# Kernel tuning notes

Measured on AMD Instinct MI355X. Metric: run time of the kernel, lower is better.

The kernel has to match this reference:

```python
import jax, jax.numpy as jnp
import numpy as np

N_DOF = 7
WIDTH = 1024
BATCH = 8192
EPS = 1e-5
LSIZE = N_DOF * (N_DOF + 1) // 2   # diag (n) + strictly-lower ((n^2-n)/2)


def _tri_idx(n):
    # order matches LowTri: offset -i chunks, within-chunk j -> entry (j+i, j)
    r, c = [], []
    for i in range(n):
        for j in range(n - i):
            r.append(j + i)
            c.append(j)
    return np.array(r, np.int32), np.array(c, np.int32)

_R, _C = _tri_idx(N_DOF)


def setup_inputs() -> dict:
    key = jax.random.key(0)
    ks = jax.random.split(key, 9)

    def glorot(k, shape):
        std = (2.0 / (shape[0] + shape[1])) ** 0.5
        return (jax.random.normal(k, shape, jnp.float32) * std).astype(jnp.float32)

    lower = LSIZE - N_DOF
    b0 = 0.1
    return {
        "state": jax.random.normal(ks[0], (BATCH, N_DOF), jnp.float32),
        "velocity": jax.random.normal(ks[1], (BATCH, N_DOF), jnp.float32),
        "acceleration": jax.random.normal(ks[2], (BATCH, N_DOF), jnp.float32),
        "W_in": glorot(ks[3], (N_DOF, WIDTH)), "b_in": jnp.full((WIDTH,), b0, jnp.float32),
        "W_h": glorot(ks[4], (WIDTH, WIDTH)), "b_h": jnp.full((WIDTH,), b0, jnp.float32),
        "W_g": glorot(ks[5], (WIDTH, 1)), "b_g": jnp.full((1,), b0, jnp.float32),
        "W_ld": glorot(ks[6], (WIDTH, N_DOF)), "b_ld": jnp.full((N_DOF,), b0, jnp.float32),
        "W_lo": glorot(ks[7], (WIDTH, lower)), "b_lo": jnp.full((lower,), b0, jnp.float32),
    }


def _layer(x, der, W, b, act):
    # a: [B, out]; der: [B, in, n_dof] -> [B, out, n_dof]
    a = x @ W + b
    if act == "relu":
        y = jax.nn.relu(a)
        gp = (a > 0).astype(a.dtype)
    else:  # linear
        y = a
        gp = jnp.ones_like(a)
    # diag(g'(a)) @ W^T @ prev_der  ==  g'(a)[:, :, None] * (W^T @ prev_der)
    new_der = gp[:, :, None] * jnp.einsum("io,bid->bod", W, der)
    return y, new_der


def _forward(state, velocity, acceleration,
             W_in, b_in, W_h, b_h, W_g, b_g, W_ld, b_ld, W_lo, b_lo):
    B = state.shape[0]
    eye = jnp.broadcast_to(jnp.eye(N_DOF, dtype=state.dtype), (B, N_DOF, N_DOF))

    y1, d1 = _layer(state, eye, W_in, b_in, "relu")
    y2, d2 = _layer(y1, d1, W_h, b_h, "relu")
    y3, d3 = _layer(y2, d2, W_h, b_h, "relu")   # original reuses hidden_layer1 twice

    V, derV = _layer(y3, d3, W_g, b_g, "linear")       # derV: [B, 1, n_dof]
    l_diag, der_ld = _layer(y3, d3, W_ld, b_ld, "relu")
    l_low, der_lo = _layer(y3, d3, W_lo, b_lo, "linear")

    l = jnp.concatenate([l_diag, l_low], axis=1)          # [B, LSIZE]
    der_l = jnp.concatenate([der_ld, der_lo], axis=1)     # [B, LSIZE, n_dof]

    def lowtri(v):   # [B, LSIZE] -> [B, n, n]
        return jnp.zeros((B, N_DOF, N_DOF), v.dtype).at[:, _R, _C].set(v)

    def lowtri3d(v):  # [B, n_dof, LSIZE] -> [B, n_dof, n, n]
        return jnp.zeros((B, N_DOF, N_DOF, N_DOF), v.dtype).at[:, :, _R, _C].set(v)

    L = lowtri(l)
    LT = jnp.swapaxes(L, 1, 2)
    M = L @ LT + EPS * jnp.eye(N_DOF, dtype=L.dtype)

    dldt = jnp.einsum("bld,bd->bl", der_l, velocity)
    dLdt = lowtri(dldt)
    dMdt = L @ jnp.swapaxes(dLdt, 1, 2) + dLdt @ LT

    dLdq = lowtri3d(jnp.swapaxes(der_l, 1, 2))            # [B, n_dof, n, n]
    dMdq = dLdq @ LT[:, None] + L[:, None] @ jnp.swapaxes(dLdq, 2, 3)

    dMdt_dq = jnp.einsum("bij,bj->bi", dMdt, velocity)
    quad_dq = jnp.einsum("bi,bkij,bj->bk", velocity, dMdq, velocity)
    C = dMdt_dq - 0.5 * quad_dq
    G = derV[:, 0, :]                                      # squeeze [B,1,n_dof]
    Mddq = jnp.einsum("bij,bj->bi", M, acceleration)
    tau_pred = Mddq + C + G
    return tau_pred, M, C, G


def reference(state, velocity, acceleration,
              W_in, b_in, W_h, b_h, W_g, b_g, W_ld, b_ld, W_lo, b_lo):
    return _forward(state, velocity, acceleration,
                    W_in, b_in, W_h, b_h, W_g, b_g, W_ld, b_ld, W_lo, b_lo)
```

## Files before the change

### kernel.cpp

```cpp
#include <hip/hip_runtime.h>
#include <hip/hip_bf16.h>

#define WIDTH 1024
#define BATCH 8192

typedef __attribute__((ext_vector_type(8))) short short8;
typedef __attribute__((ext_vector_type(4))) float floatx4;

typedef __attribute__((address_space(1))) void gvoid;
typedef __attribute__((address_space(3))) void lvoid;

__device__ __forceinline__ void async_copy16(const void* g, void* l) {
    __builtin_amdgcn_global_load_lds((gvoid*)g, (lvoid*)l, 16, 0, 0);
}

__device__ __forceinline__ void split_store(float v, __hip_bfloat16* hi, __hip_bfloat16* lo, long idx) {
    __hip_bfloat16 h = __float2bfloat16(v);
    hi[idx] = h;
    lo[idx] = __float2bfloat16(v - __bfloat162float(h));
}

__global__ __launch_bounds__(256) void transpose_k(
    const float* __restrict__ W,
    __hip_bfloat16* __restrict__ Wth, __hip_bfloat16* __restrict__ Wtl)
{
    __shared__ float t[32][33];
    const int tx = threadIdx.x & 31, ty = threadIdx.x >> 5;
    const int bx = blockIdx.x << 5, by = blockIdx.y << 5;
#pragma unroll
    for (int r = 0; r < 32; r += 8)
        t[ty + r][tx] = W[(long)(by + ty + r) * WIDTH + bx + tx];
    __syncthreads();
#pragma unroll
    for (int r = 0; r < 32; r += 8)
        split_store(t[tx][ty + r], Wth, Wtl, (long)(bx + ty + r) * WIDTH + by + tx);
}

__global__ __launch_bounds__(256) void buildwcat_k(
    const float* __restrict__ W_ld, const float* __restrict__ W_lo,
    const float* __restrict__ W_g,
    __hip_bfloat16* __restrict__ Wch, __hip_bfloat16* __restrict__ Wcl)
{
    const int idx = blockIdx.x * 256 + threadIdx.x;
    const int n = idx >> 10, k = idx & 1023;
    float v = 0.f;
    if (n < 7)       v = W_ld[k * 7 + n];
    else if (n < 28) v = W_lo[k * 21 + (n - 7)];
    else if (n == 28) v = W_g[k];
    split_store(v, Wch, Wcl, idx);
}

__global__ __launch_bounds__(256) void prep_k(
    const float* __restrict__ state,
    const float* __restrict__ W_in,
    const float* __restrict__ b_in,
    __hip_bfloat16* __restrict__ Y1h, __hip_bfloat16* __restrict__ Y1l,
    __hip_bfloat16* __restrict__ D1h)
{
    const int b = blockIdx.x;
    const int j0 = threadIdx.x * 4;
    float s[7];
#pragma unroll
    for (int d = 0; d < 7; ++d) s[d] = state[b * 7 + d];
    float a[4];
#pragma unroll
    for (int q = 0; q < 4; ++q) a[q] = b_in[j0 + q];
    float w[7][4];
#pragma unroll
    for (int d = 0; d < 7; ++d)
#pragma unroll
        for (int q = 0; q < 4; ++q) {
            w[d][q] = W_in[d * WIDTH + j0 + q];
            a[q] += s[d] * w[d][q];
        }
    bool gp[4];
#pragma unroll
    for (int q = 0; q < 4; ++q) {
        gp[q] = a[q] > 0.f;
        split_store(gp[q] ? a[q] : 0.f, Y1h, Y1l, (long)b * WIDTH + j0 + q);
    }
    union { unsigned long long u64; unsigned short h[4]; } pk;
#pragma unroll
    for (int d = 0; d < 7; ++d) {
#pragma unroll
        for (int q = 0; q < 4; ++q) {
            __hip_bfloat16 v = __float2bfloat16(gp[q] ? w[d][q] : 0.f);
            pk.h[q] = *reinterpret_cast<unsigned short*>(&v);
        }
        *reinterpret_cast<unsigned long long*>(&D1h[((long)b * 7 + d) * WIDTH + j0]) = pk.u64;
    }
}

__device__ __forceinline__ void y_gemm_body(
    short* SM,
    int bm, int bn, int tid,
    const __hip_bfloat16* Ah, const __hip_bfloat16* Al,
    const __hip_bfloat16* Bh, const __hip_bfloat16* Bl,
    const float* bias,
    __hip_bfloat16* outh, __hip_bfloat16* outl)
{
    short* Ash = SM;          short* Asl = SM + 4096;
    short* Bsh = SM + 8192;   short* Bsl = SM + 12288;
    const int lane = tid & 63;
    const int wv = tid >> 6;
    const int wm = wv >> 1, wn = wv & 1;
    const int srow = tid >> 2;
    const int scol = (tid & 3) << 3;
    const short* pAh = (const short*)Ah + (long)(bm * 128 + srow) * WIDTH + scol;
    const short* pAl = (const short*)Al + (long)(bm * 128 + srow) * WIDTH + scol;
    const short* pBh = (const short*)Bh + (long)(bn * 128 + srow) * WIDTH + scol;
    const short* pBl = (const short*)Bl + (long)(bn * 128 + srow) * WIDTH + scol;
    const long half = 64l * WIDTH;

    floatx4 acc[4][4] = {};
    const int r = lane & 15;
    const int kq = (lane >> 4) << 3;

    for (int kt = 0; kt < WIDTH; kt += 32) {
        __syncthreads();
        async_copy16(pAh + kt,        Ash + wv * 512);
        async_copy16(pAh + half + kt, Ash + 2048 + wv * 512);
        async_copy16(pAl + kt,        Asl + wv * 512);
        async_copy16(pAl + half + kt, Asl + 2048 + wv * 512);
        async_copy16(pBh + kt,        Bsh + wv * 512);
        async_copy16(pBh + half + kt, Bsh + 2048 + wv * 512);
        async_copy16(pBl + kt,        Bsl + wv * 512);
        async_copy16(pBl + half + kt, Bsl + 2048 + wv * 512);
        __syncthreads();
        short8 afh[4], afl[4], bfh[4], bfl[4];
#pragma unroll
        for (int i = 0; i < 4; ++i) {
            const int ar = (wm * 64 + i * 16 + r) * 32 + kq;
            afh[i] = *reinterpret_cast<const short8*>(&Ash[ar]);
            afl[i] = *reinterpret_cast<const short8*>(&Asl[ar]);
        }
#pragma unroll
        for (int j = 0; j < 4; ++j) {
            const int br = (wn * 64 + j * 16 + r) * 32 + kq;
            bfh[j] = *reinterpret_cast<const short8*>(&Bsh[br]);
            bfl[j] = *reinterpret_cast<const short8*>(&Bsl[br]);
        }
#pragma unroll
        for (int i = 0; i < 4; ++i)
#pragma unroll
            for (int j = 0; j < 4; ++j) {
                acc[i][j] = __builtin_amdgcn_mfma_f32_16x16x32_bf16(afh[i], bfh[j], acc[i][j], 0, 0, 0);
                acc[i][j] = __builtin_amdgcn_mfma_f32_16x16x32_bf16(afh[i], bfl[j], acc[i][j], 0, 0, 0);
                acc[i][j] = __builtin_amdgcn_mfma_f32_16x16x32_bf16(afl[i], bfh[j], acc[i][j], 0, 0, 0);
            }
    }

    const int r4 = (lane >> 4) << 2;
#pragma unroll
    for (int i = 0; i < 4; ++i)
#pragma unroll
        for (int j = 0; j < 4; ++j) {
            const int col = bn * 128 + wn * 64 + j * 16 + r;
#pragma unroll
            for (int rr = 0; rr < 4; ++rr) {
                const int row = bm * 128 + wm * 64 + i * 16 + r4 + rr;
                float v = acc[i][j][rr] + bias[col];
                v = v > 0.f ? v : 0.f;
                split_store(v, outh, outl, (long)row * WIDTH + col);
            }
        }
}

__global__ __launch_bounds__(256) void gemm_y(
    const __hip_bfloat16* __restrict__ Ah, const __hip_bfloat16* __restrict__ Al,
    const __hip_bfloat16* __restrict__ Bh, const __hip_bfloat16* __restrict__ Bl,
    const float* __restrict__ bias,
    __hip_bfloat16* __restrict__ outh, __hip_bfloat16* __restrict__ outl)
{
    __shared__ __align__(16) short SM[16384];
    y_gemm_body(SM, blockIdx.x, blockIdx.y, threadIdx.x, Ah, Al, Bh, Bl, bias, outh, outl);
}

__global__ __launch_bounds__(256) void d2y3_k(
    const __hip_bfloat16* __restrict__ D1,
    const __hip_bfloat16* __restrict__ Wth, const __hip_bfloat16* __restrict__ Wtl,
    const __hip_bfloat16* __restrict__ Y2h, const __hip_bfloat16* __restrict__ Y2l,
    const float* __restrict__ bias,
    __hip_bfloat16* __restrict__ D2out,
    __hip_bfloat16* __restrict__ Y3h, __hip_bfloat16* __restrict__ Y3l,
    int nd)
{
    __shared__ __align__(16) short SM[16384];
    const int tid = threadIdx.x;
    if ((int)blockIdx.x >= nd) {
        y_gemm_body(SM, blockIdx.x - nd, blockIdx.y, tid, Y2h, Y2l, Wth, Wtl, bias, Y3h, Y3l);
        return;
    }
    short* Ash0 = SM;         short* Ash1 = SM + 4096;
    short* Bsh0 = SM + 8192;  short* Bsh1 = SM + 12288;
    const int lane = tid & 63;
    const int wv = tid >> 6;
    const int wm = wv >> 1, wn = wv & 1;
    const int bm = blockIdx.x, bn = blockIdx.y;

    const int srow = tid >> 2;
    const int scol = (tid & 3) << 3;
    const short* pAh = (const short*)D1 + (long)(bm * 128 + srow) * WIDTH + scol;
    const short* pBh = (const short*)Wth + (long)(bn * 128 + srow) * WIDTH + scol;
    const long half = 64l * WIDTH;

    floatx4 acc[4][4] = {};
    const int r = lane & 15;
    const int kq = (lane >> 4) << 3;

    for (int kt = 0; kt < WIDTH; kt += 64) {
        __syncthreads();
        async_copy16(pAh + kt,             Ash0 + wv * 512);
        async_copy16(pAh + half + kt,      Ash0 + 2048 + wv * 512);
        async_copy16(pAh + kt + 32,        Ash1 + wv * 512);
        async_copy16(pAh + half + kt + 32, Ash1 + 2048 + wv * 512);
        async_copy16(pBh + kt,             Bsh0 + wv * 512);
        async_copy16(pBh + half + kt,      Bsh0 + 2048 + wv * 512);
        async_copy16(pBh + kt + 32,        Bsh1 + wv * 512);
        async_copy16(pBh + half + kt + 32, Bsh1 + 2048 + wv * 512);
        __syncthreads();
#pragma unroll
        for (int s = 0; s < 2; ++s) {
            const short* As = s ? Ash1 : Ash0;
            const short* Bs = s ? Bsh1 : Bsh0;
            short8 afh[4], bfh[4];
#pragma unroll
            for (int i = 0; i < 4; ++i)
                afh[i] = *reinterpret_cast<const short8*>(&As[(wm * 64 + i * 16 + r) * 32 + kq]);
#pragma unroll
            for (int j = 0; j < 4; ++j)
                bfh[j] = *reinterpret_cast<const short8*>(&Bs[(wn * 64 + j * 16 + r) * 32 + kq]);
#pragma unroll
            for (int i = 0; i < 4; ++i)
#pragma unroll
                for (int j = 0; j < 4; ++j)
                    acc[i][j] = __builtin_amdgcn_mfma_f32_16x16x32_bf16(afh[i], bfh[j], acc[i][j], 0, 0, 0);
        }
    }

    const int r4 = (lane >> 4) << 2;
#pragma unroll
    for (int i = 0; i < 4; ++i)
#pragma unroll
        for (int j = 0; j < 4; ++j) {
            const int col = bn * 128 + wn * 64 + j * 16 + r;
#pragma unroll
            for (int rr = 0; rr < 4; ++rr) {
                const int row = bm * 128 + wm * 64 + i * 16 + r4 + rr;
                float v = acc[i][j][rr];
                const unsigned brow = (unsigned)row / 7u;
                if (!(__bfloat162float(Y2h[(long)brow * WIDTH + col]) > 0.f)) v = 0.f;
                D2out[(long)row * WIDTH + col] = __float2bfloat16(v);
            }
        }
}

__global__ __launch_bounds__(256) void d3heady_k(
    const __hip_bfloat16* __restrict__ D2,
    const __hip_bfloat16* __restrict__ Wth, const __hip_bfloat16* __restrict__ Wtl,
    const __hip_bfloat16* __restrict__ Y3h, const __hip_bfloat16* __restrict__ Y3l,
    const __hip_bfloat16* __restrict__ Wch, const __hip_bfloat16* __restrict__ Wcl,
    float* __restrict__ PDpart, float* __restrict__ PY,
    int nd, int Mrows)
{
    __shared__ __align__(16) short SM[26112];
    const int tid = threadIdx.x;
    const int lane = tid & 63;
    const int wv = tid >> 6;
    const int r = lane & 15;
    const int kq = (lane >> 4) << 3;
    const int r4 = (lane >> 4) << 2;
    const int srow = tid >> 2;
    const int scol = (tid & 3) << 3;
    const long half = 64l * WIDTH;

    if ((int)blockIdx.x >= nd) {
        if (blockIdx.y != 0) return;
        short* Ash = SM;          short* Asl = SM + 4096;
        short* Bsh = SM + 8192;   short* Bsl = SM + 9216;
        const int bm = blockIdx.x - nd;
        const short* pAh = (const short*)Y3h + (long)(bm * 128 + srow) * WIDTH + scol;
        const short* pAl = (const short*)Y3l + (long)(bm * 128 + srow) * WIDTH + scol;
        const long boff = (long)srow * WIDTH + scol;
        const short* pBh = (const short*)Wch;  const short* pBl = (const short*)Wcl;

        floatx4 acc[2][2] = {};
        for (int kt = 0; kt < WIDTH; kt += 32) {
            short8 gbh, gbl;
            if (tid < 128) {
                gbh = *reinterpret_cast<const short8*>(pBh + boff + kt);
                gbl = *reinterpret_cast<const short8*>(pBl + boff + kt);
            }
            __syncthreads();
            async_copy16(pAh + kt,        Ash + wv * 512);
            async_copy16(pAh + half + kt, Ash + 2048 + wv * 512);
            async_copy16(pAl + kt,        Asl + wv * 512);
            async_copy16(pAl + half + kt, Asl + 2048 + wv * 512);
            if (tid < 128) {
                *reinterpret_cast<short8*>(&Bsh[srow * 32 + scol]) = gbh;
                *reinterpret_cast<short8*>(&Bsl[srow * 32 + scol]) = gbl;
            }
            __syncthreads();
            short8 afh[2], afl[2], bfh[2], bfl[2];
#pragma unroll
            for (int i = 0; i < 2; ++i) {
                const int ar = (wv * 32 + i * 16 + r) * 32 + kq;
                afh[i] = *reinterpret_cast<const short8*>(&Ash[ar]);
                afl[i] = *reinterpret_cast<const short8*>(&Asl[ar]);
            }
#pragma unroll
            for (int j = 0; j < 2; ++j) {
                const int br = (j * 16 + r) * 32 + kq;
                bfh[j] = *reinterpret_cast<const short8*>(&Bsh[br]);
                bfl[j] = *reinterpret_cast<const short8*>(&Bsl[br]);
            }
#pragma unroll
            for (int i = 0; i < 2; ++i)
#pragma unroll
                for (int j = 0; j < 2; ++j) {
                    acc[i][j] = __builtin_amdgcn_mfma_f32_16x16x32_bf16(afh[i], bfh[j], acc[i][j], 0, 0, 0);
                    acc[i][j] = __builtin_amdgcn_mfma_f32_16x16x32_bf16(afh[i], bfl[j], acc[i][j], 0, 0, 0);
                    acc[i][j] = __builtin_amdgcn_mfma_f32_16x16x32_bf16(afl[i], bfh[j], acc[i][j], 0, 0, 0);
                }
        }
#pragma unroll
        for (int i = 0; i < 2; ++i)
#pragma unroll
            for (int j = 0; j < 2; ++j)
#pragma unroll
                for (int rr = 0; rr < 4; ++rr) {
                    const int row = bm * 128 + wv * 32 + i * 16 + r4 + rr;
                    PY[(long)row * 32 + j * 16 + r] = acc[i][j][rr];
                }
        return;
    }

    short* Ash0 = SM;         short* Ash1 = SM + 4096;
    short* Bsh0 = SM + 8192;  short* Bsh1 = SM + 12288;
    short* T    = SM;
    short* WcH  = SM + 17408;
    short* WcL  = SM + 21760;

    const int wm = wv >> 1, wn = wv & 1;
    const int bm = blockIdx.x, bn = blockIdx.y;
    const short* pAh = (const short*)D2 + (long)(bm * 128 + srow) * WIDTH + scol;
    const short* pBh = (const short*)Wth + (long)(bn * 128 + srow) * WIDTH + scol;

    floatx4 acc[4][4] = {};
    for (int kt = 0; kt < WIDTH; kt += 64) {
        __syncthreads();
        async_copy16(pAh + kt,             Ash0 + wv * 512);
        async_copy16(pAh + half + kt,      Ash0 + 2048 + wv * 512);
        async_copy16(pAh + kt + 32,        Ash1 + wv * 512);
        async_copy16(pAh + half + kt + 32, Ash1 + 2048 + wv * 512);
        async_copy16(pBh + kt,             Bsh0 + wv * 512);
        async_copy16(pBh + half + kt,      Bsh0 + 2048 + wv * 512);
        async_copy16(pBh + kt + 32,        Bsh1 + wv * 512);
        async_copy16(pBh + half + kt + 32, Bsh1 + 2048 + wv * 512);
        __syncthreads();
#pragma unroll
        for (int s = 0; s < 2; ++s) {
            const short* As = s ? Ash1 : Ash0;
            const short* Bs = s ? Bsh1 : Bsh0;
            short8 afh[4], bfh[4];
#pragma unroll
            for (int i = 0; i < 4; ++i)
                afh[i] = *reinterpret_cast<const short8*>(&As[(wm * 64 + i * 16 + r) * 32 + kq]);
#pragma unroll
            for (int j = 0; j < 4; ++j)
                bfh[j] = *reinterpret_cast<const short8*>(&Bs[(wn * 64 + j * 16 + r) * 32 + kq]);
#pragma unroll
            for (int i = 0; i < 4; ++i)
#pragma unroll
                for (int j = 0; j < 4; ++j)
                    acc[i][j] = __builtin_amdgcn_mfma_f32_16x16x32_bf16(afh[i], bfh[j], acc[i][j], 0, 0, 0);
        }
    }

    __syncthreads();
#pragma unroll
    for (int i = 0; i < 4; ++i)
#pragma unroll
        for (int j = 0; j < 4; ++j) {
            const int coll = wn * 64 + j * 16 + r;
            const int colg = bn * 128 + coll;
#pragma unroll
            for (int rr = 0; rr < 4; ++rr) {
                const int rowl = wm * 64 + i * 16 + r4 + rr;
                const int rowg = bm * 128 + rowl;
                float v = acc[i][j][rr];
                const unsigned brow = (unsigned)rowg / 7u;
                if (!(__bfloat162float(Y3h[(long)brow * WIDTH + colg]) > 0.f)) v = 0.f;
                __hip_bfloat16 hb = __float2bfloat16(v);
                T[rowl * 136 + coll] = *reinterpret_cast<short*>(&hb);
            }
        }
    {
        const int n = tid >> 4, k8 = (tid & 15) * 8;
        const short* wh = (const short*)Wch;
        const short* wl = (const short*)Wcl;
        *reinterpret_cast<short8*>(&WcH[n * 136 + k8]) =
            *reinterpret_cast<const short8*>(wh + n * WIDTH + bn * 128 + k8);
        *reinterpret_cast<short8*>(&WcH[(n + 16) * 136 + k8]) =
            *reinterpret_cast<const short8*>(wh + (n + 16) * WIDTH + bn * 128 + k8);
        *reinterpret_cast<short8*>(&WcL[n * 136 + k8]) =
            *reinterpret_cast<const short8*>(wl + n * WIDTH + bn * 128 + k8);
        *reinterpret_cast<short8*>(&WcL[(n + 16) * 136 + k8]) =
            *reinterpret_cast<const short8*>(wl + (n + 16) * WIDTH + bn * 128 + k8);
    }
    __syncthreads();

    floatx4 accp[2][2] = {};
#pragma unroll
    for (int kk = 0; kk < 128; kk += 32) {
        short8 af[2], bh8[2], bl8[2];
#pragma unroll
        for (int i = 0; i < 2; ++i)
            af[i] = *reinterpret_cast<const short8*>(&T[(wv * 32 + i * 16 + r) * 136 + kk + kq]);
#pragma unroll
        for (int j = 0; j < 2; ++j) {
            bh8[j] = *reinterpret_cast<const short8*>(&WcH[(j * 16 + r) * 136 + kk + kq]);
            bl8[j] = *reinterpret_cast<const short8*>(&WcL[(j * 16 + r) * 136 + kk + kq]);
        }
#pragma unroll
        for (int i = 0; i < 2; ++i)
#pragma unroll
            for (int j = 0; j < 2; ++j) {
                accp[i][j] = __builtin_amdgcn_mfma_f32_16x16x32_bf16(af[i], bh8[j], accp[i][j], 0, 0, 0);
                accp[i][j] = __builtin_amdgcn_mfma_f32_16x16x32_bf16(af[i], bl8[j], accp[i][j], 0, 0, 0);
            }
    }
#pragma unroll
    for (int i = 0; i < 2; ++i)
#pragma unroll
        for (int j = 0; j < 2; ++j)
#pragma unroll
            for (int rr = 0; rr < 4; ++rr) {
                const int rowg = bm * 128 + wv * 32 + i * 16 + r4 + rr;
                PDpart[((long)bn * Mrows + rowg) * 32 + j * 16 + r] = accp[i][j][rr];
            }
}

__device__ __forceinline__ int midx(int rr, int cc) {
    const int i = rr - cc;
    return i * 7 - (i * (i - 1)) / 2 + cc;
}

__global__ __launch_bounds__(64) void finalize_k(
    const float* __restrict__ PY,
    const float* __restrict__ PDpart,
    const float* __restrict__ vel_g,
    const float* __restrict__ acc_g,
    const float* __restrict__ b_ld,
    const float* __restrict__ b_lo,
    float* __restrict__ out,
    int b0, int Mrows)
{
    __shared__ float lval[28];
    __shared__ int gpv[7];
    __shared__ float derl[29 * 7];
    __shared__ float Lm[49], Mm[49], dLt[49], uu[49];
    __shared__ float wvv[7], pv[7], Cv[7], Gv[7], tauv[7], vl[7], ac[7];

    const int bl = blockIdx.x, tid = threadIdx.x;
    const int b = b0 + bl;
    if (tid < 28) {
        float s = PY[(long)bl * 32 + tid];
        if (tid < 7) {
            s += b_ld[tid];
            gpv[tid] = s > 0.f;
            lval[tid] = s > 0.f ? s : 0.f;
        } else {
            lval[tid] = s + b_lo[tid - 7];
        }
    }
    if (tid >= 28 && tid < 35) {
        vl[tid - 28] = vel_g[b * 7 + tid - 28];
        ac[tid - 28] = acc_g[b * 7 + tid - 28];
    }
    __syncthreads();
    for (int idx = tid; idx < 203; idx += 64) {
        const int m = idx / 7, d = idx % 7;
        float v = 0.f;
#pragma unroll
        for (int p = 0; p < 8; ++p)
            v += PDpart[((long)p * Mrows + bl * 7 + d) * 32 + m];
        if (m < 7 && !gpv[m]) v = 0.f;
        derl[m * 7 + d] = v;
    }
    __syncthreads();
    if (tid < 49) {
        const int rr = tid / 7, cc = tid % 7;
        Lm[tid] = (rr >= cc) ? lval[midx(rr, cc)] : 0.f;
    }
    __syncthreads();
    if (tid < 49) {
        const int rr = tid / 7, cc = tid % 7;
        float s = 0.f;
        for (int k = 0; k < 7; ++k) s += Lm[rr * 7 + k] * Lm[cc * 7 + k];
        if (rr == cc) s += 1e-5f;
        Mm[tid] = s;
        float t = 0.f;
        if (rr >= cc) {
            const int m = midx(rr, cc);
            for (int d = 0; d < 7; ++d) t += derl[m * 7 + d] * vl[d];
        }
        dLt[tid] = t;
        float u = 0.f;
        for (int r2 = cc; r2 < 7; ++r2) u += vl[r2] * derl[midx(r2, cc) * 7 + rr];
        uu[tid] = u;
    } else if (tid >= 49 && tid < 56) {
        const int j = tid - 49;
        float s = 0.f;
        for (int r2 = 0; r2 < 7; ++r2) s += Lm[r2 * 7 + j] * vl[r2];
        wvv[j] = s;
    }
    __syncthreads();
    if (tid < 7) {
        float s = 0.f;
        for (int r2 = 0; r2 < 7; ++r2) s += dLt[r2 * 7 + tid] * vl[r2];
        pv[tid] = s;
    }
    __syncthreads();
    if (tid < 7) {
        float s = 0.f, q = 0.f, md = 0.f;
        for (int c = 0; c < 7; ++c) {
            s += Lm[tid * 7 + c] * pv[c] + dLt[tid * 7 + c] * wvv[c];
            q += uu[tid * 7 + c] * wvv[c];
            md += Mm[tid * 7 + c] * ac[c];
        }
        Cv[tid] = s - q;
        Gv[tid] = derl[28 * 7 + tid];
        tauv[tid] = md + Cv[tid] + Gv[tid];
    }
    __syncthreads();
    if (tid < 49) out[57344 + (long)b * 49 + tid] = Mm[tid];
    if (tid < 7) {
        out[(long)b * 7 + tid] = tauv[tid];
        out[458752 + (long)b * 7 + tid] = Cv[tid];
        out[516096 + (long)b * 7 + tid] = Gv[tid];
    }
}

extern "C" void kernel_launch(void* const* d_in, const int* in_sizes, int n_in,
                              void* d_out, int out_size, void* d_ws, size_t ws_size,
                              hipStream_t stream)
{
    const float* state = (const float*)d_in[0];
    const float* vel   = (const float*)d_in[1];
    const float* accel = (const float*)d_in[2];
    const float* W_in  = (const float*)d_in[3];
    const float* b_in  = (const float*)d_in[4];
    const float* W_h   = (const float*)d_in[5];
    const float* b_h   = (const float*)d_in[6];
    const float* W_g   = (const float*)d_in[7];
    const float* W_ld  = (const float*)d_in[9];
    const float* b_ld  = (const float*)d_in[10];
    const float* W_lo  = (const float*)d_in[11];
    const float* b_lo  = (const float*)d_in[12];
    float* outp = (float*)d_out;

    char* ws = (char*)d_ws;
    __hip_bfloat16* Wth = (__hip_bfloat16*)ws; ws += (size_t)WIDTH * WIDTH * 2;
    __hip_bfloat16* Wtl = (__hip_bfloat16*)ws; ws += (size_t)WIDTH * WIDTH * 2;
    __hip_bfloat16* Wch = (__hip_bfloat16*)ws; ws += 32 * WIDTH * 2;
    __hip_bfloat16* Wcl = (__hip_bfloat16*)ws; ws += 32 * WIDTH * 2;
    const size_t fixed = (size_t)(ws - (char*)d_ws);

    int CH = 128;
    for (int cand = 8192; cand >= 128; cand >>= 1) {
        size_t need = fixed + (size_t)cand * 37120;
        if (need <= ws_size) { CH = cand; break; }
    }
    const int NCH = BATCH / CH;

    const size_t YB = (size_t)CH * WIDTH * 2;
    const size_t DB = (size_t)CH * 7 * WIDTH * 2;
    __hip_bfloat16* Yah = (__hip_bfloat16*)ws; ws += YB;
    __hip_bfloat16* Yal = (__hip_bfloat16*)ws; ws += YB;
    __hip_bfloat16* Ybh = (__hip_bfloat16*)ws; ws += YB;
    __hip_bfloat16* Ybl = (__hip_bfloat16*)ws; ws += YB;
    __hip_bfloat16* Dah = (__hip_bfloat16*)ws; ws += DB;
    __hip_bfloat16* Dbh = (__hip_bfloat16*)ws; ws += DB;
    float* PY = (float*)ws; ws += (size_t)CH * 32 * 4;
    float* PDpart = (float*)Dah;

    const int Mrows = CH * 7;
    const int nd = Mrows / 128;
    const int ny = CH / 128;

    transpose_k<<<dim3(32, 32), dim3(256), 0, stream>>>(W_h, Wth, Wtl);
    buildwcat_k<<<dim3(128), dim3(256), 0, stream>>>(W_ld, W_lo, W_g, Wch, Wcl);

    for (int c = 0; c < NCH; ++c) {
        prep_k<<<dim3(CH), dim3(256), 0, stream>>>(state + (size_t)c * CH * 7, W_in, b_in,
                                                   Yah, Yal, Dah);
        gemm_y<<<dim3(ny, 8), dim3(256), 0, stream>>>(
            Yah, Yal, Wth, Wtl, b_h, Ybh, Ybl);
        d2y3_k<<<dim3(nd + ny, 8), dim3(256), 0, stream>>>(
            Dah, Wth, Wtl, Ybh, Ybl, b_h, Dbh, Yah, Yal, nd);
        d3heady_k<<<dim3(nd + ny, 8), dim3(256), 0, stream>>>(
            Dbh, Wth, Wtl, Yah, Yal, Wch, Wcl, PDpart, PY, nd, Mrows);
        finalize_k<<<dim3(CH), dim3(64), 0, stream>>>(PY, PDpart, vel, accel, b_ld, b_lo,
                                                      outp, c * CH, Mrows);
    }
    (void)in_sizes; (void)n_in; (void)out_size;
}
```

Baseline: 666.4 us.

## Load MFMA operands directly from global memory instead of staging through LDS

The two large derivative GEMMs (D1·W and D2·W) no longer copy tiles into shared memory with async global-to-LDS loads between barriers. Each wave now reads its MFMA A and B fragments straight from global memory into registers, with a k-step of 32 and a loop unrolled by 2. The aim is to drop the barrier and LDS round-trip costs. In exchange, tiles shared between waves are fetched redundantly, each lane does strided 16-byte reads, and global-load latency is exposed with only the compiler's unrolling to hide it.

```diff
diff --git a/kernel.cpp b/kernel.cpp
--- a/kernel.cpp
+++ b/kernel.cpp
@@ -191,51 +191,38 @@
         y_gemm_body(SM, blockIdx.x - nd, blockIdx.y, tid, Y2h, Y2l, Wth, Wtl, bias, Y3h, Y3l);
         return;
     }
-    short* Ash0 = SM;         short* Ash1 = SM + 4096;
-    short* Bsh0 = SM + 8192;  short* Bsh1 = SM + 12288;
     const int lane = tid & 63;
     const int wv = tid >> 6;
     const int wm = wv >> 1, wn = wv & 1;
     const int bm = blockIdx.x, bn = blockIdx.y;
-
-    const int srow = tid >> 2;
-    const int scol = (tid & 3) << 3;
-    const short* pAh = (const short*)D1 + (long)(bm * 128 + srow) * WIDTH + scol;
-    const short* pBh = (const short*)Wth + (long)(bn * 128 + srow) * WIDTH + scol;
-    const long half = 64l * WIDTH;
-
-    floatx4 acc[4][4] = {};
     const int r = lane & 15;
     const int kq = (lane >> 4) << 3;
 
-    for (int kt = 0; kt < WIDTH; kt += 64) {
-        __syncthreads();
-        async_copy16(pAh + kt,             Ash0 + wv * 512);
-        async_copy16(pAh + half + kt,      Ash0 + 2048 + wv * 512);
-        async_copy16(pAh + kt + 32,        Ash1 + wv * 512);
-        async_copy16(pAh + half + kt + 32, Ash1 + 2048 + wv * 512);
-        async_copy16(pBh + kt,             Bsh0 + wv * 512);
-        async_copy16(pBh + half + kt,      Bsh0 + 2048 + wv * 512);
-        async_copy16(pBh + kt + 32,        Bsh1 + wv * 512);
-        async_copy16(pBh + half + kt + 32, Bsh1 + 2048 + wv * 512);
-        __syncthreads();
-#pragma unroll
-        for (int s = 0; s < 2; ++s) {
-            const short* As = s ? Ash1 : Ash0;
-            const short* Bs = s ? Bsh1 : Bsh0;
-            short8 afh[4], bfh[4];
-#pragma unroll
-            for (int i = 0; i < 4; ++i)
-                afh[i] = *reinterpret_cast<const short8*>(&As[(wm * 64 + i * 16 + r) * 32 + kq]);
+    const short* A_ = (const short*)D1;
+    const short* B_ = (const short*)Wth;
+    long aoff[4], boff[4];
+#pragma unroll
+    for (int i = 0; i < 4; ++i)
+        aoff[i] = (long)(bm * 128 + wm * 64 + i * 16 + r) * WIDTH + kq;
+#pragma unroll
+    for (int j = 0; j < 4; ++j)
+        boff[j] = (long)(bn * 128 + wn * 64 + j * 16 + r) * WIDTH + kq;
+
+    floatx4 acc[4][4] = {};
+#pragma unroll 2
+    for (int kt = 0; kt < WIDTH; kt += 32) {
+        short8 a[4], b[4];
+#pragma unroll
+        for (int i = 0; i < 4; ++i)
+            a[i] = *reinterpret_cast<const short8*>(A_ + aoff[i] + kt);
+#pragma unroll
+        for (int j = 0; j < 4; ++j)
+            b[j] = *reinterpret_cast<const short8*>(B_ + boff[j] + kt);
+#pragma unroll
+        for (int i = 0; i < 4; ++i)
 #pragma unroll
             for (int j = 0; j < 4; ++j)
-                bfh[j] = *reinterpret_cast<const short8*>(&Bs[(wn * 64 + j * 16 + r) * 32 + kq]);
-#pragma unroll
-            for (int i = 0; i < 4; ++i)
-#pragma unroll
-                for (int j = 0; j < 4; ++j)
-                    acc[i][j] = __builtin_amdgcn_mfma_f32_16x16x32_bf16(afh[i], bfh[j], acc[i][j], 0, 0, 0);
-        }
+                acc[i][j] = __builtin_amdgcn_mfma_f32_16x16x32_bf16(a[i], b[j], acc[i][j], 0, 0, 0);
     }
 
     const int r4 = (lane >> 4) << 2;
@@ -335,49 +322,39 @@
         return;
     }
 
-    short* Ash0 = SM;         short* Ash1 = SM + 4096;
-    short* Bsh0 = SM + 8192;  short* Bsh1 = SM + 12288;
     short* T    = SM;
     short* WcH  = SM + 17408;
     short* WcL  = SM + 21760;
 
     const int wm = wv >> 1, wn = wv & 1;
     const int bm = blockIdx.x, bn = blockIdx.y;
-    const short* pAh = (const short*)D2 + (long)(bm * 128 + srow) * WIDTH + scol;
-    const short* pBh = (const short*)Wth + (long)(bn * 128 + srow) * WIDTH + scol;
+    const short* A_ = (const short*)D2;
+    const short* B_ = (const short*)Wth;
+    long aoff[4], boff2[4];
+#pragma unroll
+    for (int i = 0; i < 4; ++i)
+        aoff[i] = (long)(bm * 128 + wm * 64 + i * 16 + r) * WIDTH + kq;
+#pragma unroll
+    for (int j = 0; j < 4; ++j)
+        boff2[j] = (long)(bn * 128 + wn * 64 + j * 16 + r) * WIDTH + kq;
 
     floatx4 acc[4][4] = {};
-    for (int kt = 0; kt < WIDTH; kt += 64) {
-        __syncthreads();
-        async_copy16(pAh + kt,             Ash0 + wv * 512);
-        async_copy16(pAh + half + kt,      Ash0 + 2048 + wv * 512);
-        async_copy16(pAh + kt + 32,        Ash1 + wv * 512);
-        async_copy16(pAh + half + kt + 32, Ash1 + 2048 + wv * 512);
-        async_copy16(pBh + kt,             Bsh0 + wv * 512);
-        async_copy16(pBh + half + kt,      Bsh0 + 2048 + wv * 512);
-        async_copy16(pBh + kt + 32,        Bsh1 + wv * 512);
-        async_copy16(pBh + half + kt + 32, Bsh1 + 2048 + wv * 512);
-        __syncthreads();
-#pragma unroll
-        for (int s = 0; s < 2; ++s) {
-            const short* As = s ? Ash1 : Ash0;
-            const short* Bs = s ? Bsh1 : Bsh0;
-            short8 afh[4], bfh[4];
-#pragma unroll
-            for (int i = 0; i < 4; ++i)
-                afh[i] = *reinterpret_cast<const short8*>(&As[(wm * 64 + i * 16 + r) * 32 + kq]);
+#pragma unroll 2
+    for (int kt = 0; kt < WIDTH; kt += 32) {
+        short8 a[4], b[4];
+#pragma unroll
+        for (int i = 0; i < 4; ++i)
+            a[i] = *reinterpret_cast<const short8*>(A_ + aoff[i] + kt);
+#pragma unroll
+        for (int j = 0; j < 4; ++j)
+            b[j] = *reinterpret_cast<const short8*>(B_ + boff2[j] + kt);
+#pragma unroll
+        for (int i = 0; i < 4; ++i)
 #pragma unroll
             for (int j = 0; j < 4; ++j)
-                bfh[j] = *reinterpret_cast<const short8*>(&Bs[(wn * 64 + j * 16 + r) * 32 + kq]);
-#pragma unroll
-            for (int i = 0; i < 4; ++i)
-#pragma unroll
-                for (int j = 0; j < 4; ++j)
-                    acc[i][j] = __builtin_amdgcn_mfma_f32_16x16x32_bf16(afh[i], bfh[j], acc[i][j], 0, 0, 0);
-        }
-    }
-
-    __syncthreads();
+                acc[i][j] = __builtin_amdgcn_mfma_f32_16x16x32_bf16(a[i], b[j], acc[i][j], 0, 0, 0);
+    }
+
 #pragma unroll
     for (int i = 0; i < 4; ++i)
 #pragma unroll
```

After: 1.160 ms. 74.0% more time.
